# Kernel tuning notes

Measured on AMD Instinct MI355X. Metric: run time of the kernel, lower is better.

The kernel has to match this reference:

```python
import jax, jax.numpy as jnp
import numpy as np

N_LAYERS = 4
D_MODEL = 64        # 8*8 hardcoded in source
D_STATE = 128
D_CONV = 4
EXPAND = 2
HEADDIM = 64        # Mamba2Simple default
D_INNER = EXPAND * D_MODEL            # 128
NHEADS = D_INNER // HEADDIM           # 2
NGROUPS = 1
D_IN_PROJ = 2 * D_INNER + 2 * NGROUPS * D_STATE + NHEADS   # 514
CONV_DIM = D_INNER + 2 * NGROUPS * D_STATE                 # 384
EPS = 1e-5
B_SZ, SEQ = 8, 4096


def setup_inputs() -> dict:
    key = jax.random.key(0)
    ks = jax.random.split(key, 8)
    s = 0.02
    x = jax.random.normal(ks[0], (B_SZ, SEQ, D_MODEL), jnp.float32)
    in_proj_w = jax.random.normal(ks[1], (N_LAYERS, D_IN_PROJ, D_MODEL), jnp.float32) * s
    conv_w = jax.random.normal(ks[2], (N_LAYERS, CONV_DIM, 1, D_CONV), jnp.float32) * 0.2
    conv_b = jnp.zeros((N_LAYERS, CONV_DIM), jnp.float32)
    # dt_bias ~ inverse-softplus of small dt values
    dt_bias = jax.random.uniform(ks[3], (N_LAYERS, NHEADS), jnp.float32, -4.0, 0.0)
    A_log = jnp.log(jax.random.uniform(ks[4], (N_LAYERS, NHEADS), jnp.float32, 1.0, 16.0))
    D = jnp.ones((N_LAYERS, NHEADS), jnp.float32)
    norm_w = jnp.ones((N_LAYERS, D_INNER), jnp.float32)
    out_proj_w = jax.random.normal(ks[5], (N_LAYERS, D_MODEL, D_INNER), jnp.float32) * s
    return {"x": x, "in_proj_w": in_proj_w, "conv_w": conv_w, "conv_b": conv_b,
            "dt_bias": dt_bias, "A_log": A_log, "D": D, "norm_w": norm_w,
            "out_proj_w": out_proj_w}


def _ssm(xh, dt, A, Bm, Cm):
    """Selective-scan SSM. xh:(B,L,H,P) dt:(B,L,H) A:(H,) Bm,Cm:(B,L,S) -> (B,L,H,P)"""
    dA = jnp.exp(dt * A)  # (B,L,H)

    def step(h, inp):
        dA_t, dt_t, x_t, B_t, C_t = inp
        # h: (B,H,P,S)
        h = h * dA_t[:, :, None, None] + (dt_t[:, :, None] * x_t)[..., None] * B_t[:, None, None, :]
        y = jnp.einsum('bhps,bs->bhp', h, C_t)
        return h, y

    b = xh.shape[0]
    h0 = jnp.zeros((b, NHEADS, HEADDIM, D_STATE), xh.dtype)
    xs = (jnp.moveaxis(dA, 1, 0), jnp.moveaxis(dt, 1, 0), jnp.moveaxis(xh, 1, 0),
          jnp.moveaxis(Bm, 1, 0), jnp.moveaxis(Cm, 1, 0))
    _, ys = jax.lax.scan(step, h0, xs)
    return jnp.moveaxis(ys, 0, 1)


def _layer(x, p):
    in_w, cw, cb, dtb, Alog, Dp, nw, ow = p
    zxbcdt = x @ in_w.T                                   # (B,L,514)
    z = zxbcdt[..., :D_INNER]
    xBC = zxbcdt[..., D_INNER:D_INNER + CONV_DIM]
    dt = jax.nn.softplus(zxbcdt[..., -NHEADS:] + dtb)     # (B,L,H)
    # causal depthwise conv over sequence
    xc = jnp.moveaxis(xBC, -1, 1)                         # (B,C,L)
    xc = jax.lax.conv_general_dilated(xc, cw, (1,), [(D_CONV - 1, 0)],
                                      dimension_numbers=('NCH', 'OIH', 'NCH'),
                                      feature_group_count=CONV_DIM)
    xBC = jax.nn.silu(jnp.moveaxis(xc + cb[None, :, None], 1, -1))
    xs = xBC[..., :D_INNER]
    Bm = xBC[..., D_INNER:D_INNER + D_STATE]
    Cm = xBC[..., D_INNER + D_STATE:]
    xh = xs.reshape(xs.shape[0], xs.shape[1], NHEADS, HEADDIM)
    A = -jnp.exp(Alog)                                    # (H,)
    y = _ssm(xh, dt, A, Bm, Cm) + Dp[None, None, :, None] * xh
    y = y.reshape(y.shape[0], y.shape[1], D_INNER)
    # gated RMSNorm (norm_before_gate=False): rmsnorm(y * silu(z)) * w
    y = y * jax.nn.silu(z)
    y = y * jax.lax.rsqrt(jnp.mean(y * y, axis=-1, keepdims=True) + EPS) * nw
    return y @ ow.T


def reference(x, in_proj_w, conv_w, conv_b, dt_bias, A_log, D, norm_w, out_proj_w):
    def body(xc, p):
        return _layer(xc, p) + xc, None
    out, _ = jax.lax.scan(body, x, (in_proj_w, conv_w, conv_b, dt_bias, A_log, D, norm_w, out_proj_w))
    return out
```

## Files before the change

### kernel.cpp

```cpp
#include <hip/hip_runtime.h>
#include <math.h>

#define B_SZ 8
#define SEQ  4096
#define DM   64
#define DI   128
#define NH   2
#define HD   64
#define DS   128
#define DIP  514
#define XW   384
#define CD   384
#define QC   64
#define NC   64
#define NR   (B_SZ*SEQ)
#define WPAD 576

typedef __attribute__((ext_vector_type(8))) short bf16x8;
typedef __attribute__((ext_vector_type(4))) float f32x4;
typedef __attribute__((ext_vector_type(2))) __bf16 bf16x2;

__device__ __forceinline__ unsigned short f2bf(float f) {
    union { __bf16 h; unsigned short u; } x;
    x.h = (__bf16)f;
    return x.u;
}
__device__ __forceinline__ unsigned int pk2(float lo, float hi) {
    union { bf16x2 v; unsigned int u; } x;
    x.v[0] = (__bf16)lo;
    x.v[1] = (__bf16)hi;
    return x.u;
}
__device__ __forceinline__ float bf2f(unsigned short h) {
    union { unsigned int u; float f; } x; x.u = ((unsigned int)h) << 16;
    return x.f;
}
__device__ __forceinline__ bf16x8 fragld(const unsigned short* base, int r0, int k0, int ld) {
    int l = threadIdx.x & 63;
    return *(const bf16x8*)(base + (ptrdiff_t)(r0 + (l & 15)) * ld + k0 + (l >> 4) * 8);
}

__global__ __launch_bounds__(256) void k_wcvt(const float* __restrict__ in_w,
                                              const float* __restrict__ out_w,
                                              unsigned short* __restrict__ Wb,
                                              unsigned short* __restrict__ OWb) {
    int idx = blockIdx.x * 256 + threadIdx.x;
    if (idx < 4 * WPAD * 64) {
        int l = idx / (WPAD * 64), r = idx % (WPAD * 64);
        int n = r >> 6, k = r & 63;
        float v = (n < DIP) ? in_w[(size_t)l * DIP * 64 + (size_t)n * 64 + k] : 0.f;
        Wb[idx] = f2bf(v);
    }
    if (idx < 4 * 64 * 128) OWb[idx] = f2bf(out_w[idx]);
}

__global__ __launch_bounds__(256) void k_xcvt(const float* __restrict__ X,
                                              unsigned short* __restrict__ Xb) {
    int idx = (blockIdx.x * 256 + threadIdx.x) * 4;
    float4 v = *(const float4*)(X + idx);
    uint2 p;
    p.x = pk2(v.x, v.y);
    p.y = pk2(v.z, v.w);
    *(uint2*)(Xb + idx) = p;
}

__global__ __launch_bounds__(256) void k_inproj(const unsigned short* __restrict__ Xb,
                                                const unsigned short* __restrict__ Wb,
                                                unsigned short* __restrict__ ZXb,
                                                float* __restrict__ DT) {
    int m0 = blockIdx.x * 256;
    int ny = blockIdx.y;
    int tid = threadIdx.x;
    int wid = tid >> 6, lane = tid & 63;
    int q4 = lane >> 4, c16 = lane & 15;
    int mb = m0 + wid * 64;
    bf16x8 af[4][2];
#pragma unroll
    for (int mt = 0; mt < 4; mt++)
#pragma unroll
        for (int ks = 0; ks < 2; ks++)
            af[mt][ks] = *(const bf16x8*)(Xb + (size_t)(mb + mt * 16 + c16) * 64 + ks * 32 + q4 * 8);
    if (ny < 6) {
#pragma unroll
        for (int nt = 0; nt < 4; nt++) {
            bf16x8 bf[2];
#pragma unroll
            for (int ks = 0; ks < 2; ks++)
                bf[ks] = *(const bf16x8*)(Wb + (size_t)(128 + ny * 64 + nt * 16 + c16) * 64 + ks * 32 + q4 * 8);
#pragma unroll
            for (int mt = 0; mt < 4; mt++) {
                f32x4 acc = {0.f, 0.f, 0.f, 0.f};
                acc = __builtin_amdgcn_mfma_f32_16x16x32_bf16(af[mt][0], bf[0], acc, 0, 0, 0);
                acc = __builtin_amdgcn_mfma_f32_16x16x32_bf16(af[mt][1], bf[1], acc, 0, 0, 0);
#pragma unroll
                for (int rr = 0; rr < 4; rr++) {
                    float v = acc[rr];
                    float vn = __shfl_xor(v, 1);
                    if (!(lane & 1)) {
                        unsigned int pk = pk2(v, vn);
                        *(unsigned int*)(ZXb + (size_t)(mb + mt * 16 + q4 * 4 + rr) * XW + ny * 64 + nt * 16 + c16) = pk;
                    }
                }
            }
        }
    } else {
        bf16x8 bf[2];
#pragma unroll
        for (int ks = 0; ks < 2; ks++)
            bf[ks] = *(const bf16x8*)(Wb + (size_t)(512 + c16) * 64 + ks * 32 + q4 * 8);
#pragma unroll
        for (int mt = 0; mt < 4; mt++) {
            f32x4 acc = {0.f, 0.f, 0.f, 0.f};
            acc = __builtin_amdgcn_mfma_f32_16x16x32_bf16(af[mt][0], bf[0], acc, 0, 0, 0);
            acc = __builtin_amdgcn_mfma_f32_16x16x32_bf16(af[mt][1], bf[1], acc, 0, 0, 0);
            if (c16 < 2)
#pragma unroll
                for (int rr = 0; rr < 4; rr++)
                    DT[(size_t)(mb + mt * 16 + q4 * 4 + rr) * 2 + c16] = acc[rr];
        }
    }
}

__global__ __launch_bounds__(1024, 8) void k_chunk1(
        const unsigned short* __restrict__ ZXb, const float* __restrict__ DT,
        const float* __restrict__ CW, const float* __restrict__ CB,
        const float* __restrict__ dtb, const float* __restrict__ Alog,
        const float* __restrict__ Dv,
        unsigned short* __restrict__ SL, unsigned short* __restrict__ CBuf,
        float* __restrict__ EB,
        float* __restrict__ TB, unsigned short* __restrict__ YBb) {
    __shared__ unsigned short sBt[128][72];
    __shared__ unsigned short sXt[128][72];
    __shared__ unsigned short uBC[2][64][136];
    __shared__ float s_cum[2][64], s_dt[2][64], s_w[2][64];
    unsigned short (*sM)[64][72] = (unsigned short (*)[64][72])&uBC[0][0][0];

    int c = blockIdx.x, b = blockIdx.y;
    size_t rbase = (size_t)b * SEQ + c * QC;
    int tid = threadIdx.x;
    int wid = tid >> 6, lane = tid & 63;
    int q4 = lane >> 4, c16 = lane & 15;

    if (wid < 2) {
        int h = wid, j = lane;
        float raw = DT[(rbase + j) * 2 + h] + dtb[h];
        float dt = (raw > 20.f) ? raw : log1pf(__expf(raw));
        float A = -__expf(Alog[h]);
        float x = dt * A;
        for (int off = 1; off < 64; off <<= 1) {
            float o = __shfl_up(x, off);
            if (lane >= off) x += o;
        }
        float T = __shfl(x, 63);
        s_dt[h][j] = dt;
        s_cum[h][j] = x;
        s_w[h][j] = __expf(T - x) * dt;
        EB[((size_t)(b * NC + c)) * 128 + h * 64 + j] = __expf(x);
        if (j == 0) TB[(b * 2 + h) * NC + c] = __expf(T);
    }

    size_t cbbase = ((size_t)(b * NC + c)) * 8192;
    for (int e = tid; e < 64 * 96; e += 1024) {
        int j = e / 96;
        int q = e - j * 96;
        int cc = q * 4;
        int l = c * QC + j;
        const unsigned short* zp = ZXb + (rbase + j) * XW + cc;
        uint2 a0 = *(const uint2*)zp;
        uint2 a1 = make_uint2(0, 0), a2 = make_uint2(0, 0), a3 = make_uint2(0, 0);
        if (l >= 1) a1 = *(const uint2*)(zp - XW);
        if (l >= 2) a2 = *(const uint2*)(zp - 2 * XW);
        if (l >= 3) a3 = *(const uint2*)(zp - 3 * XW);
        float v[4];
#pragma unroll
        for (int u = 0; u < 4; u++) {
            unsigned int w0 = (u < 2) ? a0.x : a0.y;
            unsigned int w1 = (u < 2) ? a1.x : a1.y;
            unsigned int w2 = (u < 2) ? a2.x : a2.y;
            unsigned int w3 = (u < 2) ? a3.x : a3.y;
            int sh = (u & 1) * 16;
            float r0 = bf2f((unsigned short)(w0 >> sh));
            float r1 = bf2f((unsigned short)(w1 >> sh));
            float r2 = bf2f((unsigned short)(w2 >> sh));
            float r3 = bf2f((unsigned short)(w3 >> sh));
            float4 wv = *(const float4*)(CW + (cc + u) * 4);
            float tt = CB[cc + u] + wv.w * r0 + wv.z * r1 + wv.y * r2 + wv.x * r3;
            v[u] = tt / (1.f + __expf(-tt));
        }
        if (cc < 128) {
#pragma unroll
            for (int u = 0; u < 4; u++) sXt[cc + u][j] = f2bf(v[u]);
        } else if (cc < 256) {
            int s = cc - 128;
            unsigned int p0 = pk2(v[0], v[1]);
            unsigned int p1 = pk2(v[2], v[3]);
            *(uint2*)&uBC[0][j][s] = make_uint2(p0, p1);
#pragma unroll
            for (int u = 0; u < 4; u++) sBt[s + u][j] = f2bf(v[u]);
        } else {
            int s = cc - 256;
            unsigned int p0 = pk2(v[0], v[1]);
            unsigned int p1 = pk2(v[2], v[3]);
            *(uint2*)&uBC[1][j][s] = make_uint2(p0, p1);
            *(uint2*)(CBuf + cbbase + (size_t)j * 128 + s) = make_uint2(p0, p1);
        }
    }
    __syncthreads();

    f32x4 gacc;
    {
        int it = wid >> 2, jt = wid & 3;
        f32x4 acc = {0.f, 0.f, 0.f, 0.f};
        for (int ks = 0; ks < 4; ks++) {
            bf16x8 a = fragld(&uBC[1][0][0], it * 16, ks * 32, 136);
            bf16x8 bb = fragld(&uBC[0][0][0], jt * 16, ks * 32, 136);
            acc = __builtin_amdgcn_mfma_f32_16x16x32_bf16(a, bb, acc, 0, 0, 0);
        }
        gacc = acc;
    }
    __syncthreads();
    {
        int it = wid >> 2, jt = wid & 3;
        int j = jt * 16 + c16;
        for (int rr = 0; rr < 4; rr++) {
            int i = it * 16 + q4 * 4 + rr;
            float gv = gacc[rr];
            for (int h = 0; h < 2; h++) {
                float m = 0.f;
                if (j <= i) m = gv * __expf(s_cum[h][i] - s_cum[h][j]) * s_dt[h][j];
                sM[h][i][j] = f2bf(m);
            }
        }
    }
    __syncthreads();

    size_t ybase = ((size_t)(b * NC + c)) * 8192;
#pragma unroll
    for (int u = 0; u < 2; u++) {
        int idx = wid * 2 + u;
        int h = idx >> 4, tt = idx & 15;
        int it = tt >> 2, pt = tt & 3;
        float dco = Dv[h];
        int pg = h * 64 + pt * 16 + c16;
        f32x4 acc;
        for (int rr = 0; rr < 4; rr++) {
            int i = it * 16 + q4 * 4 + rr;
            acc[rr] = dco * bf2f(sXt[pg][i]);
        }
        for (int ks = 0; ks < 2; ks++) {
            bf16x8 a = fragld(&sM[h][0][0], it * 16, ks * 32, 72);
            bf16x8 bb = fragld(&sXt[0][0], h * 64 + pt * 16, ks * 32, 72);
            acc = __builtin_amdgcn_mfma_f32_16x16x32_bf16(a, bb, acc, 0, 0, 0);
        }
        uint2 pk;
        pk.x = pk2(acc[0], acc[1]);
        pk.y = pk2(acc[2], acc[3]);
        *(uint2*)(YBb + ybase + (size_t)idx * 256 + lane * 4) = pk;
    }
    __syncthreads();
    {
        int row = tid >> 3, c0 = (tid & 7) * 8;
        uint4 xv = *(uint4*)&sXt[row][c0];
        const float* wp = s_w[row >> 6];
        unsigned int* px = &xv.x;
        uint4 ov;
        unsigned int* po = &ov.x;
#pragma unroll
        for (int t = 0; t < 4; t++) {
            float lo = bf2f((unsigned short)(px[t] & 0xffff)) * wp[c0 + 2 * t];
            float hi = bf2f((unsigned short)(px[t] >> 16)) * wp[c0 + 2 * t + 1];
            po[t] = pk2(lo, hi);
        }
        *(uint4*)&sXt[row][c0] = ov;
    }
    __syncthreads();
    size_t slbase = ((size_t)(b * NC + c)) * 16384;
#pragma unroll
    for (int u = 0; u < 4; u++) {
        int idx = wid * 4 + u;
        int ptl = idx >> 3, st = idx & 7;
        f32x4 acc = {0.f, 0.f, 0.f, 0.f};
        for (int ks = 0; ks < 2; ks++) {
            bf16x8 a = fragld(&sXt[0][0], ptl * 16, ks * 32, 72);
            bf16x8 bb = fragld(&sBt[0][0], st * 16, ks * 32, 72);
            acc = __builtin_amdgcn_mfma_f32_16x16x32_bf16(a, bb, acc, 0, 0, 0);
        }
        int s = st * 16 + c16;
        for (int rr = 0; rr < 4; rr++) {
            int p = ptl * 16 + q4 * 4 + rr;
            float vv = acc[rr];
            float vn = __shfl_xor(vv, 1);
            if (!(lane & 1)) {
                unsigned int pk = pk2(vv, vn);
                *(unsigned int*)(SL + slbase + (size_t)p * 128 + s) = pk;
            }
        }
    }
}

__global__ __launch_bounds__(256) void k_scan(unsigned short* __restrict__ SL,
                                              const float* __restrict__ TB) {
    int bid = blockIdx.x;
    int b = bid >> 5;
    int pu = (bid & 31) * 256 + threadIdx.x;
    int h = pu >> 12;
    const float* dAp = TB + (b * 2 + h) * NC;
    size_t base = (size_t)(b * NC) * 16384 + (size_t)pu * 2;
    float h0 = 0.f, h1 = 0.f;
#pragma unroll 8
    for (int cc = 0; cc < NC; cc++) {
        size_t idx = base + (size_t)cc * 16384;
        unsigned int v = *(unsigned int*)(SL + idx);
        float s0 = bf2f((unsigned short)(v & 0xffff));
        float s1 = bf2f((unsigned short)(v >> 16));
        *(unsigned int*)(SL + idx) = pk2(h0, h1);
        float dA = dAp[cc];
        h0 = h0 * dA + s0;
        h1 = h1 * dA + s1;
    }
}

__global__ __launch_bounds__(1024, 8) void k_fused(
        const unsigned short* __restrict__ SL, const unsigned short* __restrict__ CBuf,
        const float* __restrict__ EB,
        const unsigned short* __restrict__ YBb, const unsigned short* __restrict__ Wzb,
        const float* __restrict__ NW, const unsigned short* __restrict__ OWb,
        unsigned short* __restrict__ Xb, float* __restrict__ OutF,
        const unsigned short* __restrict__ WbN,
        unsigned short* __restrict__ ZXbO,
        float* __restrict__ DTO,
        int last) {
    __shared__ __attribute__((aligned(16))) unsigned short sH[128][136];
    __shared__ __attribute__((aligned(16))) unsigned short sE[128][136];
    float* sGf = (float*)&sH[0][0];
    unsigned short (*sG)[136] = (unsigned short (*)[136])&sE[0][0];
    unsigned short (*sX2)[72] = (unsigned short (*)[72])&sH[0][0];

    int c = blockIdx.x, b = blockIdx.y;
    size_t rbase = (size_t)b * SEQ + c * QC;
    int tid = threadIdx.x;
    int wid = tid >> 6, lane = tid & 63;
    size_t base = ((size_t)(b * NC + c)) * 16384;
    for (int u = 0; u < 2; u++) {
        int e = u * 1024 + tid;
        int row = e >> 4, cb8 = (e & 15) * 8;
        *(uint4*)&sH[row][cb8] = *(const uint4*)(SL + base + (size_t)row * 128 + cb8);
    }
    size_t cbbase = ((size_t)(b * NC + c)) * 8192;
    size_t ebase  = ((size_t)(b * NC + c)) * 128;
    {
        int i = tid >> 4, sc = (tid & 15) * 8;
        uint4 cv = *(const uint4*)(CBuf + cbbase + (size_t)i * 128 + sc);
        float e0 = EB[ebase + i], e1 = EB[ebase + 64 + i];
        unsigned int w[4] = {cv.x, cv.y, cv.z, cv.w};
        uint4 o0, o1;
        unsigned int* po0 = &o0.x;
        unsigned int* po1 = &o1.x;
#pragma unroll
        for (int t = 0; t < 4; t++) {
            float lo = bf2f((unsigned short)(w[t] & 0xffff));
            float hi = bf2f((unsigned short)(w[t] >> 16));
            po0[t] = pk2(lo * e0, hi * e0);
            po1[t] = pk2(lo * e1, hi * e1);
        }
        *(uint4*)&sE[i][sc] = o0;
        *(uint4*)&sE[64 + i][sc] = o1;
    }
    __syncthreads();
    int q4 = lane >> 4, c16 = lane & 15;

    float yv[2][4];
    int tit[2], tpg[2];
    size_t ybase = ((size_t)(b * NC + c)) * 8192;
#pragma unroll
    for (int u = 0; u < 2; u++) {
        int idx = wid * 2 + u;
        int h = idx >> 4, tt = idx & 15;
        int it = tt >> 2, pt = tt & 3;
        int pg = h * 64 + pt * 16 + c16;
        f32x4 zacc = {0.f, 0.f, 0.f, 0.f};
        f32x4 acc = {0.f, 0.f, 0.f, 0.f};
#pragma unroll
        for (int ks = 0; ks < 2; ks++) {
            bf16x8 xa = fragld(Xb, (int)rbase + it * 16, ks * 32, 64);
            bf16x8 wz = fragld(Wzb, h * 64 + pt * 16, ks * 32, 64);
            zacc = __builtin_amdgcn_mfma_f32_16x16x32_bf16(xa, wz, zacc, 0, 0, 0);
        }
        for (int ks = 0; ks < 4; ks++) {
            bf16x8 a = fragld(&sE[0][0], h * 64 + it * 16, ks * 32, 136);
            bf16x8 bb = fragld(&sH[0][0], h * 64 + pt * 16, ks * 32, 136);
            acc = __builtin_amdgcn_mfma_f32_16x16x32_bf16(a, bb, acc, 0, 0, 0);
        }
        tit[u] = it; tpg[u] = pg;
        uint2 yi = *(const uint2*)(YBb + ybase + (size_t)idx * 256 + lane * 4);
        float yin[4] = {bf2f((unsigned short)(yi.x & 0xffff)), bf2f((unsigned short)(yi.x >> 16)),
                        bf2f((unsigned short)(yi.y & 0xffff)), bf2f((unsigned short)(yi.y >> 16))};
        for (int rr = 0; rr < 4; rr++) {
            float y = acc[rr] + yin[rr];
            float z = zacc[rr];
            yv[u][rr] = y * (z / (1.f + __expf(-z)));
        }
    }
    __syncthreads();
#pragma unroll
    for (int u = 0; u < 2; u++)
        for (int rr = 0; rr < 4; rr++) {
            int i = tit[u] * 16 + q4 * 4 + rr;
            sGf[i * 132 + tpg[u]] = yv[u][rr];
        }
    __syncthreads();
    {
        int row = tid >> 4, part = tid & 15;
        int d0 = part * 8;
        float g[8];
        float ss = 0.f;
        for (int t2 = 0; t2 < 8; t2++) { g[t2] = sGf[row * 132 + d0 + t2]; ss += g[t2] * g[t2]; }
        ss += __shfl_xor(ss, 1);
        ss += __shfl_xor(ss, 2);
        ss += __shfl_xor(ss, 4);
        ss += __shfl_xor(ss, 8);
        float rms = rsqrtf(ss * (1.f / 128.f) + 1e-5f);
        for (int t2 = 0; t2 < 8; t2 += 2) {
            unsigned int pk = pk2(g[t2] * rms * NW[d0 + t2], g[t2 + 1] * rms * NW[d0 + t2 + 1]);
            *(unsigned int*)&sG[row][d0 + t2] = pk;
        }
    }
    __syncthreads();
    {
        int mt = wid >> 2, nt = wid & 3;
        f32x4 acc = {0.f, 0.f, 0.f, 0.f};
        for (int ks = 0; ks < 4; ks++) {
            bf16x8 a = fragld(&sG[0][0], mt * 16, ks * 32, 136);
            bf16x8 bb = *(const bf16x8*)(OWb + (size_t)(nt * 16 + c16) * 128 + ks * 32 + q4 * 8);
            acc = __builtin_amdgcn_mfma_f32_16x16x32_bf16(a, bb, acc, 0, 0, 0);
        }
        for (int rr = 0; rr < 4; rr++) {
            int m = mt * 16 + q4 * 4 + rr;
            int n = nt * 16 + c16;
            size_t o = (rbase + m) * DM + n;
            float v = bf2f(Xb[o]) + acc[rr];
            if (last) {
                OutF[o] = v;
            } else {
                unsigned short vb = f2bf(v);
                sX2[m][n] = vb;
                float vn = __shfl_xor(v, 1);
                if (!(lane & 1)) {
                    unsigned int pk = (unsigned int)vb | ((unsigned int)f2bf(vn) << 16);
                    *(unsigned int*)(Xb + o) = pk;
                }
            }
        }
    }
    if (!last) {
        __syncthreads();
        for (int t = wid; t < 100; t += 16) {
            int mt2, n0;
            int isdt = (t >= 96);
            if (!isdt) { mt2 = t & 3; n0 = (t >> 2) * 16; }
            else       { mt2 = t - 96; n0 = 0; }
            bf16x8 a0 = fragld(&sX2[0][0], mt2 * 16, 0, 72);
            bf16x8 a1 = fragld(&sX2[0][0], mt2 * 16, 32, 72);
            const unsigned short* wrow = isdt ? (WbN + (size_t)(512 + c16) * 64)
                                              : (WbN + (size_t)(128 + n0 + c16) * 64);
            bf16x8 b0 = *(const bf16x8*)(wrow + q4 * 8);
            bf16x8 b1 = *(const bf16x8*)(wrow + 32 + q4 * 8);
            f32x4 acc = {0.f, 0.f, 0.f, 0.f};
            acc = __builtin_amdgcn_mfma_f32_16x16x32_bf16(a0, b0, acc, 0, 0, 0);
            acc = __builtin_amdgcn_mfma_f32_16x16x32_bf16(a1, b1, acc, 0, 0, 0);
            if (!isdt) {
#pragma unroll
                for (int rr = 0; rr < 4; rr++) {
                    float v = acc[rr];
                    float vn = __shfl_xor(v, 1);
                    if (!(lane & 1)) {
                        unsigned int pk = pk2(v, vn);
                        *(unsigned int*)(ZXbO + (rbase + mt2 * 16 + q4 * 4 + rr) * XW + n0 + c16) = pk;
                    }
                }
            } else {
                if (c16 < 2)
#pragma unroll
                    for (int rr = 0; rr < 4; rr++)
                        DTO[(rbase + mt2 * 16 + q4 * 4 + rr) * 2 + c16] = acc[rr];
            }
        }
    }
}

extern "C" void kernel_launch(void* const* d_in, const int* in_sizes, int n_in,
                              void* d_out, int out_size, void* d_ws, size_t ws_size,
                              hipStream_t stream) {
    const float* x       = (const float*)d_in[0];
    const float* in_w    = (const float*)d_in[1];
    const float* conv_w  = (const float*)d_in[2];
    const float* conv_b  = (const float*)d_in[3];
    const float* dt_bias = (const float*)d_in[4];
    const float* A_log   = (const float*)d_in[5];
    const float* Dp      = (const float*)d_in[6];
    const float* norm_w  = (const float*)d_in[7];
    const float* out_w   = (const float*)d_in[8];
    float* out = (float*)d_out;
    float* ws  = (float*)d_ws;

    float* dt = ws;
    float* tb = dt + (size_t)NR * 2;
    float* eb = tb + 1024;
    unsigned short* zxb  = (unsigned short*)(eb + (size_t)B_SZ * NC * 128);
    unsigned short* ybb  = zxb + (size_t)NR * XW;
    unsigned short* sl   = ybb + (size_t)B_SZ * NC * 8192;
    unsigned short* cbuf = sl + (size_t)B_SZ * NC * 16384;
    unsigned short* xb   = cbuf + (size_t)B_SZ * NC * 8192;
    unsigned short* wb   = xb + (size_t)NR * DM;
    unsigned short* owb  = wb + (size_t)4 * WPAD * 64;

    k_wcvt<<<(4 * WPAD * 64 + 255) / 256, 256, 0, stream>>>(in_w, out_w, wb, owb);
    k_xcvt<<<NR * DM / 1024, 256, 0, stream>>>(x, xb);
    k_inproj<<<dim3(NR / 256, 7), 256, 0, stream>>>(xb, wb, zxb, dt);

    for (int layer = 0; layer < 4; layer++) {
        int nl = (layer < 3) ? layer + 1 : 3;
        k_chunk1<<<dim3(NC, B_SZ), 1024, 0, stream>>>(zxb, dt,
                conv_w + (size_t)layer * CD * 4, conv_b + (size_t)layer * CD,
                dt_bias + layer * NH, A_log + layer * NH, Dp + layer * NH,
                sl, cbuf, eb, tb, ybb);
        k_scan<<<256, 256, 0, stream>>>(sl, tb);
        k_fused<<<dim3(NC, B_SZ), 1024, 0, stream>>>(sl, cbuf, eb, ybb,
                wb + (size_t)layer * WPAD * 64, norm_w + layer * DI,
                owb + (size_t)layer * 64 * 128, xb, out,
                wb + (size_t)nl * WPAD * 64, zxb, dt,
                (layer == 3) ? 1 : 0);
    }
}
```

Measured before the change: 350.3 us.

## Parallelize inter-chunk scan, merge prep kernels, add MFMA priority and prefetch

```diff
diff --git a/kernel.cpp b/kernel.cpp
--- a/kernel.cpp
+++ b/kernel.cpp
@@ -35,33 +35,38 @@
     union { unsigned int u; float f; } x; x.u = ((unsigned int)h) << 16;
     return x.f;
 }
+__device__ __forceinline__ float fsilu(float x) {
+    return x * __builtin_amdgcn_rcpf(1.f + __expf(-x));
+}
 __device__ __forceinline__ bf16x8 fragld(const unsigned short* base, int r0, int k0, int ld) {
     int l = threadIdx.x & 63;
     return *(const bf16x8*)(base + (ptrdiff_t)(r0 + (l & 15)) * ld + k0 + (l >> 4) * 8);
 }
 
-__global__ __launch_bounds__(256) void k_wcvt(const float* __restrict__ in_w,
-                                              const float* __restrict__ out_w,
-                                              unsigned short* __restrict__ Wb,
-                                              unsigned short* __restrict__ OWb) {
-    int idx = blockIdx.x * 256 + threadIdx.x;
-    if (idx < 4 * WPAD * 64) {
-        int l = idx / (WPAD * 64), r = idx % (WPAD * 64);
-        int n = r >> 6, k = r & 63;
-        float v = (n < DIP) ? in_w[(size_t)l * DIP * 64 + (size_t)n * 64 + k] : 0.f;
-        Wb[idx] = f2bf(v);
-    }
-    if (idx < 4 * 64 * 128) OWb[idx] = f2bf(out_w[idx]);
-}
-
-__global__ __launch_bounds__(256) void k_xcvt(const float* __restrict__ X,
-                                              unsigned short* __restrict__ Xb) {
-    int idx = (blockIdx.x * 256 + threadIdx.x) * 4;
-    float4 v = *(const float4*)(X + idx);
-    uint2 p;
-    p.x = pk2(v.x, v.y);
-    p.y = pk2(v.z, v.w);
-    *(uint2*)(Xb + idx) = p;
+__global__ __launch_bounds__(256) void k_pre(const float* __restrict__ in_w,
+                                             const float* __restrict__ out_w,
+                                             const float* __restrict__ X,
+                                             unsigned short* __restrict__ Wb,
+                                             unsigned short* __restrict__ OWb,
+                                             unsigned short* __restrict__ Xb) {
+    int bid = blockIdx.x;
+    if (bid < 576) {
+        int idx = bid * 256 + threadIdx.x;
+        if (idx < 4 * WPAD * 64) {
+            int l = idx / (WPAD * 64), r = idx % (WPAD * 64);
+            int n = r >> 6, k = r & 63;
+            float v = (n < DIP) ? in_w[(size_t)l * DIP * 64 + (size_t)n * 64 + k] : 0.f;
+            Wb[idx] = f2bf(v);
+        }
+        if (idx < 4 * 64 * 128) OWb[idx] = f2bf(out_w[idx]);
+    } else {
+        int idx = ((bid - 576) * 256 + threadIdx.x) * 4;
+        float4 v = *(const float4*)(X + idx);
+        uint2 p;
+        p.x = pk2(v.x, v.y);
+        p.y = pk2(v.z, v.w);
+        *(uint2*)(Xb + idx) = p;
+    }
 }
 
 __global__ __launch_bounds__(256) void k_inproj(const unsigned short* __restrict__ Xb,
@@ -185,7 +190,7 @@
             float r3 = bf2f((unsigned short)(w3 >> sh));
             float4 wv = *(const float4*)(CW + (cc + u) * 4);
             float tt = CB[cc + u] + wv.w * r0 + wv.z * r1 + wv.y * r2 + wv.x * r3;
-            v[u] = tt / (1.f + __expf(-tt));
+            v[u] = fsilu(tt);
         }
         if (cc < 128) {
 #pragma unroll
@@ -211,11 +216,13 @@
     {
         int it = wid >> 2, jt = wid & 3;
         f32x4 acc = {0.f, 0.f, 0.f, 0.f};
+        __builtin_amdgcn_s_setprio(1);
         for (int ks = 0; ks < 4; ks++) {
             bf16x8 a = fragld(&uBC[1][0][0], it * 16, ks * 32, 136);
             bf16x8 bb = fragld(&uBC[0][0][0], jt * 16, ks * 32, 136);
             acc = __builtin_amdgcn_mfma_f32_16x16x32_bf16(a, bb, acc, 0, 0, 0);
         }
+        __builtin_amdgcn_s_setprio(0);
         gacc = acc;
     }
     __syncthreads();
@@ -247,11 +254,13 @@
             int i = it * 16 + q4 * 4 + rr;
             acc[rr] = dco * bf2f(sXt[pg][i]);
         }
+        __builtin_amdgcn_s_setprio(1);
         for (int ks = 0; ks < 2; ks++) {
             bf16x8 a = fragld(&sM[h][0][0], it * 16, ks * 32, 72);
             bf16x8 bb = fragld(&sXt[0][0], h * 64 + pt * 16, ks * 32, 72);
             acc = __builtin_amdgcn_mfma_f32_16x16x32_bf16(a, bb, acc, 0, 0, 0);
         }
+        __builtin_amdgcn_s_setprio(0);
         uint2 pk;
         pk.x = pk2(acc[0], acc[1]);
         pk.y = pk2(acc[2], acc[3]);
@@ -280,11 +289,13 @@
         int idx = wid * 4 + u;
         int ptl = idx >> 3, st = idx & 7;
         f32x4 acc = {0.f, 0.f, 0.f, 0.f};
+        __builtin_amdgcn_s_setprio(1);
         for (int ks = 0; ks < 2; ks++) {
             bf16x8 a = fragld(&sXt[0][0], ptl * 16, ks * 32, 72);
             bf16x8 bb = fragld(&sBt[0][0], st * 16, ks * 32, 72);
             acc = __builtin_amdgcn_mfma_f32_16x16x32_bf16(a, bb, acc, 0, 0, 0);
         }
+        __builtin_amdgcn_s_setprio(0);
         int s = st * 16 + c16;
         for (int rr = 0; rr < 4; rr++) {
             int p = ptl * 16 + q4 * 4 + rr;
@@ -298,25 +309,48 @@
     }
 }
 
-__global__ __launch_bounds__(256) void k_scan(unsigned short* __restrict__ SL,
-                                              const float* __restrict__ TB) {
-    int bid = blockIdx.x;
-    int b = bid >> 5;
-    int pu = (bid & 31) * 256 + threadIdx.x;
-    int h = pu >> 12;
-    const float* dAp = TB + (b * 2 + h) * NC;
-    size_t base = (size_t)(b * NC) * 16384 + (size_t)pu * 2;
+__global__ __launch_bounds__(1024) void k_scan(unsigned short* __restrict__ SL,
+                                               const float* __restrict__ TB) {
+    __shared__ float sT0[8][128], sT1[8][128], sP[8];
+    int tid = threadIdx.x;
+    int col = tid & 127, seg = tid >> 7;
+    int colg = blockIdx.x * 128 + col;
+    int b2 = colg >> 13;
+    int pu = colg & 8191;
+    int h2 = pu >> 12;
+    const float* dAp = TB + (b2 * 2 + h2) * NC;
+    size_t cbase = (size_t)(b2 * NC) * 16384 + (size_t)pu * 2;
+    int cc0 = seg * 8;
+    unsigned int sv[8];
+    float dA[8];
+    float hP = 1.f, t0 = 0.f, t1 = 0.f;
+#pragma unroll
+    for (int k = 0; k < 8; k++) {
+        sv[k] = *(unsigned int*)(SL + cbase + (size_t)(cc0 + k) * 16384);
+        dA[k] = dAp[cc0 + k];
+        float sx0 = bf2f((unsigned short)(sv[k] & 0xffff));
+        float sx1 = bf2f((unsigned short)(sv[k] >> 16));
+        t0 = t0 * dA[k] + sx0;
+        t1 = t1 * dA[k] + sx1;
+        hP *= dA[k];
+    }
+    sT0[seg][col] = t0;
+    sT1[seg][col] = t1;
+    if (col == 0) sP[seg] = hP;
+    __syncthreads();
     float h0 = 0.f, h1 = 0.f;
-#pragma unroll 8
-    for (int cc = 0; cc < NC; cc++) {
-        size_t idx = base + (size_t)cc * 16384;
-        unsigned int v = *(unsigned int*)(SL + idx);
-        float s0 = bf2f((unsigned short)(v & 0xffff));
-        float s1 = bf2f((unsigned short)(v >> 16));
-        *(unsigned int*)(SL + idx) = pk2(h0, h1);
-        float dA = dAp[cc];
-        h0 = h0 * dA + s0;
-        h1 = h1 * dA + s1;
+    for (int s2 = 0; s2 < seg; s2++) {
+        float Ps = sP[s2];
+        h0 = h0 * Ps + sT0[s2][col];
+        h1 = h1 * Ps + sT1[s2][col];
+    }
+#pragma unroll
+    for (int k = 0; k < 8; k++) {
+        *(unsigned int*)(SL + cbase + (size_t)(cc0 + k) * 16384) = pk2(h0, h1);
+        float sx0 = bf2f((unsigned short)(sv[k] & 0xffff));
+        float sx1 = bf2f((unsigned short)(sv[k] >> 16));
+        h0 = h0 * dA[k] + sx0;
+        h1 = h1 * dA[k] + sx1;
     }
 }
 
@@ -340,7 +374,22 @@
     size_t rbase = (size_t)b * SEQ + c * QC;
     int tid = threadIdx.x;
     int wid = tid >> 6, lane = tid & 63;
+    int q4 = lane >> 4, c16 = lane & 15;
     size_t base = ((size_t)(b * NC + c)) * 16384;
+    size_t ybase = ((size_t)(b * NC + c)) * 8192;
+
+    uint2 yi[2];
+    bf16x8 xa[2][2];
+#pragma unroll
+    for (int u = 0; u < 2; u++) {
+        int idx = wid * 2 + u;
+        int it = (idx & 15) >> 2;
+        yi[u] = *(const uint2*)(YBb + ybase + (size_t)idx * 256 + lane * 4);
+#pragma unroll
+        for (int ks = 0; ks < 2; ks++)
+            xa[u][ks] = fragld(Xb, (int)rbase + it * 16, ks * 32, 64);
+    }
+
     for (int u = 0; u < 2; u++) {
         int e = u * 1024 + tid;
         int row = e >> 4, cb8 = (e & 15) * 8;
@@ -367,11 +416,9 @@
         *(uint4*)&sE[64 + i][sc] = o1;
     }
     __syncthreads();
-    int q4 = lane >> 4, c16 = lane & 15;
 
     float yv[2][4];
     int tit[2], tpg[2];
-    size_t ybase = ((size_t)(b * NC + c)) * 8192;
 #pragma unroll
     for (int u = 0; u < 2; u++) {
         int idx = wid * 2 + u;
@@ -380,25 +427,24 @@
         int pg = h * 64 + pt * 16 + c16;
         f32x4 zacc = {0.f, 0.f, 0.f, 0.f};
         f32x4 acc = {0.f, 0.f, 0.f, 0.f};
+        __builtin_amdgcn_s_setprio(1);
 #pragma unroll
         for (int ks = 0; ks < 2; ks++) {
-            bf16x8 xa = fragld(Xb, (int)rbase + it * 16, ks * 32, 64);
             bf16x8 wz = fragld(Wzb, h * 64 + pt * 16, ks * 32, 64);
-            zacc = __builtin_amdgcn_mfma_f32_16x16x32_bf16(xa, wz, zacc, 0, 0, 0);
+            zacc = __builtin_amdgcn_mfma_f32_16x16x32_bf16(xa[u][ks], wz, zacc, 0, 0, 0);
         }
         for (int ks = 0; ks < 4; ks++) {
             bf16x8 a = fragld(&sE[0][0], h * 64 + it * 16, ks * 32, 136);
             bf16x8 bb = fragld(&sH[0][0], h * 64 + pt * 16, ks * 32, 136);
             acc = __builtin_amdgcn_mfma_f32_16x16x32_bf16(a, bb, acc, 0, 0, 0);
         }
+        __builtin_amdgcn_s_setprio(0);
         tit[u] = it; tpg[u] = pg;
-        uint2 yi = *(const uint2*)(YBb + ybase + (size_t)idx * 256 + lane * 4);
-        float yin[4] = {bf2f((unsigned short)(yi.x & 0xffff)), bf2f((unsigned short)(yi.x >> 16)),
-                        bf2f((unsigned short)(yi.y & 0xffff)), bf2f((unsigned short)(yi.y >> 16))};
+        float yin[4] = {bf2f((unsigned short)(yi[u].x & 0xffff)), bf2f((unsigned short)(yi[u].x >> 16)),
+                        bf2f((unsigned short)(yi[u].y & 0xffff)), bf2f((unsigned short)(yi[u].y >> 16))};
         for (int rr = 0; rr < 4; rr++) {
             float y = acc[rr] + yin[rr];
-            float z = zacc[rr];
-            yv[u][rr] = y * (z / (1.f + __expf(-z)));
+            yv[u][rr] = y * fsilu(zacc[rr]);
         }
     }
     __syncthreads();
@@ -429,11 +475,13 @@
     {
         int mt = wid >> 2, nt = wid & 3;
         f32x4 acc = {0.f, 0.f, 0.f, 0.f};
+        __builtin_amdgcn_s_setprio(1);
         for (int ks = 0; ks < 4; ks++) {
             bf16x8 a = fragld(&sG[0][0], mt * 16, ks * 32, 136);
             bf16x8 bb = *(const bf16x8*)(OWb + (size_t)(nt * 16 + c16) * 128 + ks * 32 + q4 * 8);
             acc = __builtin_amdgcn_mfma_f32_16x16x32_bf16(a, bb, acc, 0, 0, 0);
         }
+        __builtin_amdgcn_s_setprio(0);
         for (int rr = 0; rr < 4; rr++) {
             int m = mt * 16 + q4 * 4 + rr;
             int n = nt * 16 + c16;
@@ -466,8 +514,10 @@
             bf16x8 b0 = *(const bf16x8*)(wrow + q4 * 8);
             bf16x8 b1 = *(const bf16x8*)(wrow + 32 + q4 * 8);
             f32x4 acc = {0.f, 0.f, 0.f, 0.f};
+            __builtin_amdgcn_s_setprio(1);
             acc = __builtin_amdgcn_mfma_f32_16x16x32_bf16(a0, b0, acc, 0, 0, 0);
             acc = __builtin_amdgcn_mfma_f32_16x16x32_bf16(a1, b1, acc, 0, 0, 0);
+            __builtin_amdgcn_s_setprio(0);
             if (!isdt) {
 #pragma unroll
                 for (int rr = 0; rr < 4; rr++) {
@@ -514,8 +564,7 @@
     unsigned short* wb   = xb + (size_t)NR * DM;
     unsigned short* owb  = wb + (size_t)4 * WPAD * 64;
 
-    k_wcvt<<<(4 * WPAD * 64 + 255) / 256, 256, 0, stream>>>(in_w, out_w, wb, owb);
-    k_xcvt<<<NR * DM / 1024, 256, 0, stream>>>(x, xb);
+    k_pre<<<576 + NR * DM / 1024, 256, 0, stream>>>(in_w, out_w, x, wb, owb, xb);
     k_inproj<<<dim3(NR / 256, 7), 256, 0, stream>>>(xb, wb, zxb, dt);
 
     for (int layer = 0; layer < 4; layer++) {
@@ -524,7 +573,7 @@
                 conv_w + (size_t)layer * CD * 4, conv_b + (size_t)layer * CD,
                 dt_bias + layer * NH, A_log + layer * NH, Dp + layer * NH,
                 sl, cbuf, eb, tb, ybb);
-        k_scan<<<256, 256, 0, stream>>>(sl, tb);
+        k_scan<<<512, 1024, 0, stream>>>(sl, tb);
         k_fused<<<dim3(NC, B_SZ), 1024, 0, stream>>>(sl, cbuf, eb, ybb,
                 wb + (size_t)layer * WPAD * 64, norm_w + layer * DI,
                 owb + (size_t)layer * 64 * 128, xb, out,
```

Result: faster. 337.5 us, median of 2 (-3.7%).
